# Kernel optimization log

Hardware: AMD Instinct MI355X
Metric: run time of the kernel (lower is better)

Reference implementation:

```python
import jax, jax.numpy as jnp
import numpy as np

NUM_HEADS = 8
D_HEAD = 16
RY = RX = 2
PH = 2 * RY + 1
PW = 2 * RX + 1
P = PH * PW  # 25 spatial positions per patch


def setup_inputs() -> dict:
    key = jax.random.key(0)
    ks = jax.random.split(key, 7)
    B, T, H, W, C = 1, 3, 96, 96, 128
    Ck = NUM_HEADS * D_HEAD
    w = lambda k, shp: jax.random.normal(k, shp, jnp.float32) * 0.05
    return {
        "x": jax.random.normal(ks[0], (B, T, H, W, C), jnp.float32),
        "Wq": w(ks[1], (C, Ck)),
        "Wk": w(ks[2], (C, Ck)),
        "Wv": w(ks[3], (C, Ck)),
        "Wo": w(ks[4], (Ck, C)),
        "temp_emb": w(ks[5], (T, Ck)),
        "sp_emb": w(ks[6], (P, Ck)),
    }


def _neighbor_idx(N, r):
    # Edge handling: patch center is clipped into the valid interior, matching
    # extract_patches(VALID) + gather_nd with clipped indices in the original.
    c = jnp.clip(jnp.arange(N), r, N - r - 1)
    return c[:, None] + jnp.arange(-r, r + 1)[None, :]  # (N, 2r+1)


def _query_spatial_idx(H, W):
    # Position of each query pixel inside its (clipped) patch.
    yc = jnp.clip(jnp.arange(H), RY, H - RY - 1)
    xc = jnp.clip(jnp.arange(W), RX, W - RX - 1)
    yr = jnp.arange(H) - yc + RY  # (H,)
    xr = jnp.arange(W) - xc + RX  # (W,)
    return yr[:, None] * PW + xr[None, :]  # (H, W) in [0, P)


def reference(x, Wq, Wk, Wv, Wo, temp_emb, sp_emb):
    B, T, H, W, C = x.shape
    h, d = NUM_HEADS, D_HEAD
    Ck = h * d
    # 1x1 conv projections (no bias) == channel matmuls
    Q = jnp.einsum('bqyxc,ck->bqyxk', x, Wq)
    K = jnp.einsum('bqyxc,ck->bqyxk', x, Wk)
    V = jnp.einsum('bqyxc,ck->bqyxk', x, Wv)
    # positional encodings added AFTER projection (attention space)
    K = K + temp_emb[None, :, None, None, :]
    qidx = _query_spatial_idx(H, W)  # (H, W)
    Q = Q + temp_emb[None, :, None, None, :] + sp_emb[qidx][None, None]
    # local spatial patch extraction with clipped-edge handling
    ynb = _neighbor_idx(H, RY)  # (H, PH)
    xnb = _neighbor_idx(W, RX)  # (W, PW)
    Kp = K[:, :, ynb[:, None, :, None], xnb[None, :, None, :], :]  # (B,T,H,W,PH,PW,Ck)
    Vp = V[:, :, ynb[:, None, :, None], xnb[None, :, None, :], :]
    Kp = Kp.reshape(B, T, H, W, P, Ck) + sp_emb[None, None, None, None]
    Vp = Vp.reshape(B, T, H, W, P, Ck)
    # merge key time into the neighborhood axis: (B,H,W,T*P,h,d)
    Kn = Kp.transpose(0, 2, 3, 1, 4, 5).reshape(B, H, W, T * P, h, d)
    Vn = Vp.transpose(0, 2, 3, 1, 4, 5).reshape(B, H, W, T * P, h, d)
    Qh = Q.reshape(B, T, H, W, h, d)
    scale = 1.0 / jnp.sqrt(jnp.asarray(d, x.dtype))
    scores = jnp.einsum('bqyxnd,byxknd->bqyxnk', Qh, Kn) * scale
    attn = jax.nn.softmax(scores, axis=-1)  # over T*P neighborhood
    out = jnp.einsum('bqyxnk,byxknd->bqyxnd', attn, Vn).reshape(B, T, H, W, Ck)
    out = jnp.einsum('bqyxk,kc->bqyxc', out, Wo)  # output 1x1 conv
    # return_list=False -> concatenate the T outputs along channels
    return out.transpose(0, 2, 3, 1, 4).reshape(B, H, W, T * C)
```

## Files before the change

kernel.cpp:

```cpp
#include <hip/hip_runtime.h>
#include <hip/hip_bf16.h>
#include <math.h>

#define TT 3
#define HH 96
#define WWD 96
#define CCH 128
#define NROWS (TT*HH*WWD)

typedef __attribute__((ext_vector_type(8))) short short8;
typedef __attribute__((ext_vector_type(4))) short short4v;
typedef __attribute__((ext_vector_type(4))) float float4v;

__device__ __forceinline__ float bfu(unsigned short u){ union{unsigned u;float f;}c; c.u=((unsigned)u)<<16; return c.f; }
__device__ __forceinline__ unsigned short f2bf(float f){ __hip_bfloat16 h=__float2bfloat16(f); return *(unsigned short*)&h; }

#if defined(__has_builtin)
#if __has_builtin(__builtin_amdgcn_mfma_f32_16x16x16bf16_1k)
#define MFMA16(A,B,C) __builtin_amdgcn_mfma_f32_16x16x16bf16_1k(A,B,C,0,0,0)
#endif
#endif
#ifndef MFMA16
static __device__ __forceinline__ float4v mfma16_asm(short4v a, short4v b, float4v c){
    float4v d;
    asm("v_mfma_f32_16x16x16_bf16 %0, %1, %2, %3" : "=v"(d) : "v"(a), "v"(b), "v"(c));
    return d;
}
#define MFMA16(A,B,C) mfma16_asm(A,B,C)
#endif

__launch_bounds__(256)
__global__ void prep_kernel(const float* __restrict__ Wq, const float* __restrict__ Wk,
                            const float* __restrict__ Wv, const float* __restrict__ Wo,
                            unsigned short* __restrict__ Wt, unsigned short* __restrict__ Wo1,
                            unsigned short* __restrict__ Wo2) {
    __shared__ float ts[32][33];
    const int m = blockIdx.x >> 4, tile = blockIdx.x & 15;
    const int k0 = (tile >> 2) * 32, n0 = (tile & 3) * 32;
    const float* src = (m == 0) ? Wq : (m == 1) ? Wk : (m == 2) ? Wv : Wo;
    const int tid = threadIdx.x;
    const int c = tid & 31, r8 = tid >> 5;
#pragma unroll
    for (int rr = 0; rr < 4; ++rr) {
        int r = r8 * 4 + rr;
        ts[r][c] = src[(size_t)(k0 + r) * 128 + n0 + c];
    }
    __syncthreads();
#pragma unroll
    for (int rr = 0; rr < 4; ++rr) {
        int r = r8 * 4 + rr;
        float v = ts[c][r];
        if (m < 3) {
            Wt[(size_t)(m * 128 + n0 + r) * 128 + k0 + c] = f2bf(v);
        } else {
            unsigned short w1 = f2bf(v);
            Wo1[(size_t)(n0 + r) * 128 + k0 + c] = w1;
            Wo2[(size_t)(n0 + r) * 128 + k0 + c] = f2bf(v - bfu(w1));
        }
    }
}

__launch_bounds__(256)
__global__ void qkv_kernel(const float* __restrict__ x,
                           const unsigned short* __restrict__ Wt,
                           const float* __restrict__ temp_emb,
                           const float* __restrict__ sp_emb,
                           unsigned short* __restrict__ Qb,
                           unsigned short* __restrict__ Kb,
                           unsigned short* __restrict__ Vb) {
    __shared__ unsigned short xs[32 * 136];
    const int tid = threadIdx.x;
    const int q0 = blockIdx.x * 32;
    for (int e = tid; e < 1024; e += 256) {
        int row = e >> 5, col = (e & 31) * 4;
        float4 v = *(const float4*)(x + (size_t)(q0 + row) * CCH + col);
        ushort4 u; u.x = f2bf(v.x); u.y = f2bf(v.y); u.z = f2bf(v.z); u.w = f2bf(v.w);
        *(ushort4*)&xs[row * 136 + col] = u;
    }
    __syncthreads();
    const int w = tid >> 6, lane = tid & 63, quad = lane >> 4, l16 = lane & 15;
    float4v acc[6][2];
#pragma unroll
    for (int mt = 0; mt < 6; ++mt)
#pragma unroll
        for (int nt = 0; nt < 2; ++nt) acc[mt][nt] = (float4v){0,0,0,0};
#pragma unroll
    for (int ks = 0; ks < 4; ++ks) {
        short8 b[2];
#pragma unroll
        for (int nt = 0; nt < 2; ++nt)
            b[nt] = *(const short8*)&xs[(nt * 16 + l16) * 136 + ks * 32 + quad * 8];
#pragma unroll
        for (int mt = 0; mt < 6; ++mt) {
            short8 a = *(const short8*)(Wt + (size_t)(w * 96 + mt * 16 + l16) * CCH + ks * 32 + quad * 8);
#pragma unroll
            for (int nt = 0; nt < 2; ++nt)
                acc[mt][nt] = __builtin_amdgcn_mfma_f32_16x16x32_bf16(a, b[nt], acc[mt][nt], 0, 0, 0);
        }
    }
#pragma unroll
    for (int nt = 0; nt < 2; ++nt) {
        int q = q0 + nt * 16 + l16;
        int t = q / (HH * WWD); int rem = q - t * (HH * WWD);
        int yy = rem / WWD, xx = rem - (rem / WWD) * WWD;
        int qidx = (yy - min(max(yy, 2), 93) + 2) * 5 + (xx - min(max(xx, 2), 93) + 2);
#pragma unroll
        for (int mt = 0; mt < 6; ++mt) {
            int colc = w * 96 + mt * 16 + quad * 4;
            int mat = colc >> 7, colb = colc & 127;
            float4v a = acc[mt][nt];
            ushort4 u;
            if (mat == 0) {
                float4 te = *(const float4*)(temp_emb + t * CCH + colb);
                float4 se = *(const float4*)(sp_emb + qidx * CCH + colb);
                u.x = f2bf((a[0] + te.x + se.x) * 0.25f);
                u.y = f2bf((a[1] + te.y + se.y) * 0.25f);
                u.z = f2bf((a[2] + te.z + se.z) * 0.25f);
                u.w = f2bf((a[3] + te.w + se.w) * 0.25f);
                *(ushort4*)(Qb + (size_t)q * CCH + colb) = u;
            } else if (mat == 1) {
                float4 te = *(const float4*)(temp_emb + t * CCH + colb);
                u.x = f2bf(a[0] + te.x); u.y = f2bf(a[1] + te.y);
                u.z = f2bf(a[2] + te.z); u.w = f2bf(a[3] + te.w);
                *(ushort4*)(Kb + (size_t)q * CCH + colb) = u;
            } else {
                u.x = f2bf(a[0]); u.y = f2bf(a[1]); u.z = f2bf(a[2]); u.w = f2bf(a[3]);
                *(ushort4*)(Vb + (size_t)q * CCH + colb) = u;
            }
        }
    }
}

#define PX 4
#define WIN 8

__launch_bounds__(512, 4)
__global__ void attn_kernel(const unsigned short* __restrict__ Qb,
                            const unsigned short* __restrict__ Kb,
                            const unsigned short* __restrict__ Vb,
                            const float* __restrict__ sp_emb,
                            const unsigned short* __restrict__ Wo1,
                            const unsigned short* __restrict__ Wo2,
                            float* __restrict__ out) {
    __shared__ unsigned short Ks[64 * 136];
    __shared__ unsigned short Vt[128 * 68];
    __shared__ float biasL[8 * 3 * 25 * 17];

    const int tid = threadIdx.x;
    const int lane = tid & 63;
    const int w = tid >> 6;
    const int quad = lane >> 4, l16 = lane & 15;
    const int h16 = w * 16;

    const int bx = blockIdx.x % (WWD / PX);
    const int by = blockIdx.x / (WWD / PX);
    const int x0 = bx * PX, y0 = by * PX;
    const int xlo = min(max(x0 - 2, 0), WWD - WIN);
    const int ylo = min(max(y0 - 2, 0), HH - WIN);

    const int qdy = l16 >> 2, qdx = l16 & 3;
    const int yy = y0 + qdy, xx = x0 + qdx;
    const int yc = min(max(yy, 2), HH - 3), xc = min(max(xx, 2), WWD - 3);

    short4v qfr[3];
#pragma unroll
    for (int qt = 0; qt < 3; ++qt) {
        int qrow = qt * (HH * WWD) + yy * WWD + xx;
        qfr[qt] = *(const short4v*)(Qb + (size_t)qrow * CCH + h16 + quad * 4);
    }

    short4v sph[2], spl[2];
#pragma unroll
    for (int tile = 0; tile < 2; ++tile) {
        int kcr = min(tile * 16 + l16, 24);
        float4 v = *(const float4*)(sp_emb + (size_t)kcr * CCH + h16 + quad * 4);
        float vv[4] = {v.x, v.y, v.z, v.w};
        union { short4v s4; unsigned short u[4]; } ph, pl;
#pragma unroll
        for (int i = 0; i < 4; ++i) {
            ph.u[i] = f2bf(vv[i]);
            pl.u[i] = f2bf(vv[i] - bfu(ph.u[i]));
        }
        sph[tile] = ph.s4; spl[tile] = pl.s4;
    }

    const int bbase = w * (3 * 25 * 17);
#pragma unroll
    for (int qt = 0; qt < 3; ++qt) {
#pragma unroll
        for (int tile = 0; tile < 2; ++tile) {
            float4v d = MFMA16(spl[tile], qfr[qt], ((float4v){0.f,0.f,0.f,0.f}));
            d = MFMA16(sph[tile], qfr[qt], d);
#pragma unroll
            for (int r = 0; r < 4; ++r) {
                int kc = tile * 16 + quad * 4 + r;
                if (kc < 25) biasL[bbase + (qt * 25 + kc) * 17 + l16] = d[r];
            }
        }
    }

    int badr[16];
#pragma unroll
    for (int kt = 0; kt < 4; ++kt)
#pragma unroll
        for (int r = 0; r < 4; ++r) {
            int slot = kt * 16 + quad * 4 + r;
            int gy = ylo + (slot >> 3), gx = xlo + (slot & 7);
            int py = gy - yc + 2, px = gx - xc + 2;
            bool ok = (py >= 0) && (py < 5) && (px >= 0) && (px < 5);
            badr[kt * 4 + r] = ok ? (bbase + (py * 5 + px) * 17 + l16) : -1;
        }

    float m[3] = {-1e30f, -1e30f, -1e30f};
    float l[3] = {0.f, 0.f, 0.f};
    float4v oacc[3];
#pragma unroll
    for (int qt = 0; qt < 3; ++qt) oacc[qt] = (float4v){0.f,0.f,0.f,0.f};

    for (int t = 0; t < TT; ++t) {
        __syncthreads();
        for (int e = tid; e < 1024; e += 512) {
            int slot = e >> 4, c = e & 15;
            int gy = ylo + (slot >> 3), gx = xlo + (slot & 7);
            size_t g = ((size_t)(t * HH + gy) * WWD + gx) * CCH + c * 8;
            *(uint4*)&Ks[slot * 136 + c * 8] = *(const uint4*)(Kb + g);
        }
        for (int p = tid; p < 1024; p += 512) {
            int sp2 = p & 31, cq = p >> 5;
            int slot0 = sp2 * 2, ch0 = cq * 4;
            int gy = ylo + (slot0 >> 3), gx = xlo + (slot0 & 7);
            size_t g = ((size_t)(t * HH + gy) * WWD + gx) * CCH + ch0;
            uint2 a = *(const uint2*)(Vb + g);
            uint2 b = *(const uint2*)(Vb + g + CCH);
            unsigned v0 = (a.x & 0xffffu) | (b.x << 16);
            unsigned v1 = (a.x >> 16)     | (b.x & 0xffff0000u);
            unsigned v2 = (a.y & 0xffffu) | (b.y << 16);
            unsigned v3 = (a.y >> 16)     | (b.y & 0xffff0000u);
            *(unsigned*)&Vt[(ch0 + 0) * 68 + slot0] = v0;
            *(unsigned*)&Vt[(ch0 + 1) * 68 + slot0] = v1;
            *(unsigned*)&Vt[(ch0 + 2) * 68 + slot0] = v2;
            *(unsigned*)&Vt[(ch0 + 3) * 68 + slot0] = v3;
        }
        __syncthreads();

        short4v kfr[4], vfr[4];
#pragma unroll
        for (int kt = 0; kt < 4; ++kt) {
            kfr[kt] = *(const short4v*)&Ks[(kt * 16 + l16) * 136 + h16 + quad * 4];
            vfr[kt] = *(const short4v*)&Vt[(h16 + l16) * 68 + kt * 16 + quad * 4];
        }

#pragma unroll
        for (int qt = 0; qt < 3; ++qt) {
            float4v s[4];
#pragma unroll
            for (int kt = 0; kt < 4; ++kt) {
                float4v c;
#pragma unroll
                for (int r = 0; r < 4; ++r) {
                    int a = badr[kt * 4 + r];
                    c[r] = (a < 0) ? -1e30f : biasL[a + qt * 425];
                }
                s[kt] = MFMA16(kfr[kt], qfr[qt], c);
            }
            float mx = m[qt];
#pragma unroll
            for (int kt = 0; kt < 4; ++kt)
#pragma unroll
                for (int r = 0; r < 4; ++r) mx = fmaxf(mx, s[kt][r]);
            mx = fmaxf(mx, __shfl_xor(mx, 16));
            mx = fmaxf(mx, __shfl_xor(mx, 32));
            float corr = __expf(m[qt] - mx);
            m[qt] = mx;
            l[qt] *= corr;
            float4v oc = oacc[qt] * corr;
            float lsum = 0.f;
            short4v pfr[4];
#pragma unroll
            for (int kt = 0; kt < 4; ++kt) {
                float p0 = __expf(s[kt][0] - mx), p1 = __expf(s[kt][1] - mx);
                float p2 = __expf(s[kt][2] - mx), p3 = __expf(s[kt][3] - mx);
                lsum += (p0 + p1) + (p2 + p3);
                union { short4v s4; unsigned short u[4]; } pk;
                pk.u[0] = f2bf(p0); pk.u[1] = f2bf(p1);
                pk.u[2] = f2bf(p2); pk.u[3] = f2bf(p3);
                pfr[kt] = pk.s4;
            }
            l[qt] += lsum;
#pragma unroll
            for (int kt = 0; kt < 4; ++kt) oc = MFMA16(vfr[kt], pfr[kt], oc);
            oacc[qt] = oc;
        }
    }

    __syncthreads();
    unsigned short* Os = Ks;
#pragma unroll
    for (int qt = 0; qt < 3; ++qt) {
        float lt = l[qt];
        lt += __shfl_xor(lt, 16);
        lt += __shfl_xor(lt, 32);
        float inv = 1.f / lt;
        union { ushort4 u4; unsigned short u[4]; } ob;
#pragma unroll
        for (int r = 0; r < 4; ++r) ob.u[r] = f2bf(oacc[qt][r] * inv);
        *(ushort4*)&Os[(qt * 16 + l16) * 136 + h16 + quad * 4] = ob.u4;
    }
    __syncthreads();

    float4v pacc[3];
#pragma unroll
    for (int nt = 0; nt < 3; ++nt) pacc[nt] = (float4v){0.f, 0.f, 0.f, 0.f};
#pragma unroll
    for (int ks = 0; ks < 4; ++ks) {
        short8 bfrag[3];
#pragma unroll
        for (int nt = 0; nt < 3; ++nt)
            bfrag[nt] = *(const short8*)&Os[(nt * 16 + l16) * 136 + ks * 32 + quad * 8];
        size_t wo = (size_t)(w * 16 + l16) * CCH + ks * 32 + quad * 8;
        short8 a1 = *(const short8*)(Wo1 + wo);
        short8 a2 = *(const short8*)(Wo2 + wo);
#pragma unroll
        for (int nt = 0; nt < 3; ++nt) {
            pacc[nt] = __builtin_amdgcn_mfma_f32_16x16x32_bf16(a1, bfrag[nt], pacc[nt], 0, 0, 0);
            pacc[nt] = __builtin_amdgcn_mfma_f32_16x16x32_bf16(a2, bfrag[nt], pacc[nt], 0, 0, 0);
        }
    }
#pragma unroll
    for (int nt = 0; nt < 3; ++nt) {
        size_t ob = ((size_t)(yy * WWD + xx) * TT + nt) * CCH;
        float4 o;
        o.x = pacc[nt][0]; o.y = pacc[nt][1]; o.z = pacc[nt][2]; o.w = pacc[nt][3];
        *(float4*)(out + ob + w * 16 + quad * 4) = o;
    }
}

extern "C" void kernel_launch(void* const* d_in, const int* in_sizes, int n_in,
                              void* d_out, int out_size, void* d_ws, size_t ws_size,
                              hipStream_t stream) {
    const float* x        = (const float*)d_in[0];
    const float* Wq       = (const float*)d_in[1];
    const float* Wk       = (const float*)d_in[2];
    const float* Wv       = (const float*)d_in[3];
    const float* Wo       = (const float*)d_in[4];
    const float* temp_emb = (const float*)d_in[5];
    const float* sp_emb   = (const float*)d_in[6];
    float* out = (float*)d_out;

    const size_t nb = (size_t)NROWS * CCH * 2;
    unsigned short* Qb  = (unsigned short*)d_ws;
    unsigned short* Kb  = (unsigned short*)((char*)d_ws + nb);
    unsigned short* Vb  = (unsigned short*)((char*)d_ws + 2 * nb);
    unsigned short* Wt  = (unsigned short*)((char*)d_ws + 3 * nb);
    unsigned short* Wo1 = Wt + 384 * 128;
    unsigned short* Wo2 = Wo1 + 128 * 128;

    prep_kernel<<<64, 256, 0, stream>>>(Wq, Wk, Wv, Wo, Wt, Wo1, Wo2);
    qkv_kernel<<<NROWS / 32, 256, 0, stream>>>(x, Wt, temp_emb, sp_emb, Qb, Kb, Vb);
    attn_kernel<<<(HH / PX) * (WWD / PX), 512, 0, stream>>>(Qb, Kb, Vb, sp_emb, Wo1, Wo2, out);
}
```

Baseline: 144.8 us.

## Load K fragments directly from global and use per-wave V transpose slabs

K MFMA fragments are now read straight from global memory by each wave instead of being staged through a block-wide shared tile. The V transpose moves into per-wave, per-head shared slabs, double-buffered by time step. That removes both block-level __syncthreads per time step, and the time loop is fully unrolled. In exchange each wave issues more scattered global loads, and correctness relies on intra-wave ordering of the slab writes and reads with no explicit barrier.

```diff
diff --git a/kernel.cpp b/kernel.cpp
--- a/kernel.cpp
+++ b/kernel.cpp
@@ -133,6 +133,8 @@
 
 #define PX 4
 #define WIN 8
+#define VSTR 68
+#define VSLAB (16*VSTR)
 
 __launch_bounds__(512, 4)
 __global__ void attn_kernel(const unsigned short* __restrict__ Qb,
@@ -142,9 +144,10 @@
                             const unsigned short* __restrict__ Wo1,
                             const unsigned short* __restrict__ Wo2,
                             float* __restrict__ out) {
-    __shared__ unsigned short Ks[64 * 136];
-    __shared__ unsigned short Vt[128 * 68];
-    __shared__ float biasL[8 * 3 * 25 * 17];
+    __shared__ __align__(16) char smem[40800 + 2 * 8 * VSLAB * 2];
+    float* biasL = (float*)smem;
+    unsigned short* VtA = (unsigned short*)(smem + 40800);
+    unsigned short* Os  = (unsigned short*)(smem + 40800);
 
     const int tid = threadIdx.x;
     const int lane = tid & 63;
@@ -217,38 +220,41 @@
 #pragma unroll
     for (int qt = 0; qt < 3; ++qt) oacc[qt] = (float4v){0.f,0.f,0.f,0.f};
 
+#pragma unroll
     for (int t = 0; t < TT; ++t) {
-        __syncthreads();
-        for (int e = tid; e < 1024; e += 512) {
-            int slot = e >> 4, c = e & 15;
+        short4v kfr[4];
+#pragma unroll
+        for (int kt = 0; kt < 4; ++kt) {
+            int slot = kt * 16 + l16;
             int gy = ylo + (slot >> 3), gx = xlo + (slot & 7);
-            size_t g = ((size_t)(t * HH + gy) * WWD + gx) * CCH + c * 8;
-            *(uint4*)&Ks[slot * 136 + c * 8] = *(const uint4*)(Kb + g);
-        }
-        for (int p = tid; p < 1024; p += 512) {
-            int sp2 = p & 31, cq = p >> 5;
-            int slot0 = sp2 * 2, ch0 = cq * 4;
+            size_t g = ((size_t)(t * HH + gy) * WWD + gx) * CCH + h16 + quad * 4;
+            kfr[kt] = *(const short4v*)(Kb + g);
+        }
+
+        unsigned short* vt = VtA + ((size_t)((t & 1) * 8 + w)) * VSLAB;
+#pragma unroll
+        for (int r = 0; r < 2; ++r) {
+            int task = r * 64 + lane;
+            int sp2 = task & 31, c4 = task >> 5;
+            int slot0 = sp2 * 2, ch0 = c4 * 4;
             int gy = ylo + (slot0 >> 3), gx = xlo + (slot0 & 7);
-            size_t g = ((size_t)(t * HH + gy) * WWD + gx) * CCH + ch0;
+            size_t g = ((size_t)(t * HH + gy) * WWD + gx) * CCH + h16 + ch0;
             uint2 a = *(const uint2*)(Vb + g);
             uint2 b = *(const uint2*)(Vb + g + CCH);
             unsigned v0 = (a.x & 0xffffu) | (b.x << 16);
             unsigned v1 = (a.x >> 16)     | (b.x & 0xffff0000u);
             unsigned v2 = (a.y & 0xffffu) | (b.y << 16);
             unsigned v3 = (a.y >> 16)     | (b.y & 0xffff0000u);
-            *(unsigned*)&Vt[(ch0 + 0) * 68 + slot0] = v0;
-            *(unsigned*)&Vt[(ch0 + 1) * 68 + slot0] = v1;
-            *(unsigned*)&Vt[(ch0 + 2) * 68 + slot0] = v2;
-            *(unsigned*)&Vt[(ch0 + 3) * 68 + slot0] = v3;
-        }
-        __syncthreads();
-
-        short4v kfr[4], vfr[4];
-#pragma unroll
-        for (int kt = 0; kt < 4; ++kt) {
-            kfr[kt] = *(const short4v*)&Ks[(kt * 16 + l16) * 136 + h16 + quad * 4];
-            vfr[kt] = *(const short4v*)&Vt[(h16 + l16) * 68 + kt * 16 + quad * 4];
-        }
+            *(unsigned*)&vt[(ch0 + 0) * VSTR + slot0] = v0;
+            *(unsigned*)&vt[(ch0 + 1) * VSTR + slot0] = v1;
+            *(unsigned*)&vt[(ch0 + 2) * VSTR + slot0] = v2;
+            *(unsigned*)&vt[(ch0 + 3) * VSTR + slot0] = v3;
+        }
+
+        short4v vfr[4];
+#pragma unroll
+        for (int kt = 0; kt < 4; ++kt)
+            vfr[kt] = *(const short4v*)&vt[l16 * VSTR + kt * 16 + quad * 4];
 
 #pragma unroll
         for (int qt = 0; qt < 3; ++qt) {
@@ -294,7 +300,6 @@
     }
 
     __syncthreads();
-    unsigned short* Os = Ks;
 #pragma unroll
     for (int qt = 0; qt < 3; ++qt) {
         float lt = l[qt];
```

Result: slower. 200.4 us (+38.4%).

## Double-buffer K/V tiles across time steps and hoist attention bias into registers

Applied to the files above, without the earlier changes.

The attention kernel now prefetches the next time step's K and V neighborhood into registers while the current step computes. It then writes them into a second LDS buffer, so each time step needs one barrier instead of two. The positional bias for all three query times is gathered from LDS into registers once, before the loop, rather than being re-read from LDS inside each score MFMA. The bias, staging and output buffers now share one aliased LDS allocation, which is smaller than before. The register-resident bias and prefetch values add a lot of register pressure under launch_bounds(512,4), which risks spills or reduced occupancy.

```diff
diff --git a/kernel.cpp b/kernel.cpp
--- a/kernel.cpp
+++ b/kernel.cpp
@@ -133,6 +133,8 @@
 
 #define PX 4
 #define WIN 8
+#define KHS 8704
+#define VHS 8704
 
 __launch_bounds__(512, 4)
 __global__ void attn_kernel(const unsigned short* __restrict__ Qb,
@@ -142,9 +144,11 @@
                             const unsigned short* __restrict__ Wo1,
                             const unsigned short* __restrict__ Wo2,
                             float* __restrict__ out) {
-    __shared__ unsigned short Ks[64 * 136];
-    __shared__ unsigned short Vt[128 * 68];
-    __shared__ float biasL[8 * 3 * 25 * 17];
+    __shared__ __align__(16) char smem[2 * KHS * 2 + 2 * VHS * 2];
+    unsigned short* KsA = (unsigned short*)smem;
+    unsigned short* VtA = (unsigned short*)(smem + 2 * KHS * 2);
+    float* biasL = (float*)smem;
+    unsigned short* Os = (unsigned short*)smem;
 
     const int tid = threadIdx.x;
     const int lane = tid & 63;
@@ -162,6 +166,55 @@
     const int yy = y0 + qdy, xx = x0 + qdx;
     const int yc = min(max(yy, 2), HH - 3), xc = min(max(xx, 2), WWD - 3);
 
+    uint4 kreg[2];
+    uint2 var[2], vbr[2];
+
+    auto stage_load = [&](int t) {
+#pragma unroll
+        for (int i = 0; i < 2; ++i) {
+            int e = i * 512 + tid;
+            int slot = e >> 4, c = e & 15;
+            int gy = ylo + (slot >> 3), gx = xlo + (slot & 7);
+            size_t g = ((size_t)(t * HH + gy) * WWD + gx) * CCH + c * 8;
+            kreg[i] = *(const uint4*)(Kb + g);
+        }
+#pragma unroll
+        for (int i = 0; i < 2; ++i) {
+            int p = i * 512 + tid;
+            int sp2 = p & 31, cq = p >> 5;
+            int slot0 = sp2 * 2;
+            int gy = ylo + (slot0 >> 3), gx = xlo + (slot0 & 7);
+            size_t g = ((size_t)(t * HH + gy) * WWD + gx) * CCH + cq * 4;
+            var[i] = *(const uint2*)(Vb + g);
+            vbr[i] = *(const uint2*)(Vb + g + CCH);
+        }
+    };
+    auto stage_write = [&](unsigned short* Kd, unsigned short* Vd) {
+#pragma unroll
+        for (int i = 0; i < 2; ++i) {
+            int e = i * 512 + tid;
+            int slot = e >> 4, c = e & 15;
+            *(uint4*)&Kd[slot * 136 + c * 8] = kreg[i];
+        }
+#pragma unroll
+        for (int i = 0; i < 2; ++i) {
+            int p = i * 512 + tid;
+            int sp2 = p & 31, cq = p >> 5;
+            int slot0 = sp2 * 2, ch0 = cq * 4;
+            uint2 a = var[i], b = vbr[i];
+            unsigned v0 = (a.x & 0xffffu) | (b.x << 16);
+            unsigned v1 = (a.x >> 16)     | (b.x & 0xffff0000u);
+            unsigned v2 = (a.y & 0xffffu) | (b.y << 16);
+            unsigned v3 = (a.y >> 16)     | (b.y & 0xffff0000u);
+            *(unsigned*)&Vd[(ch0 + 0) * 68 + slot0] = v0;
+            *(unsigned*)&Vd[(ch0 + 1) * 68 + slot0] = v1;
+            *(unsigned*)&Vd[(ch0 + 2) * 68 + slot0] = v2;
+            *(unsigned*)&Vd[(ch0 + 3) * 68 + slot0] = v3;
+        }
+    };
+
+    stage_load(0);
+
     short4v qfr[3];
 #pragma unroll
     for (int qt = 0; qt < 3; ++qt) {
@@ -199,7 +252,7 @@
         }
     }
 
-    int badr[16];
+    float4v cbias[3][4];
 #pragma unroll
     for (int kt = 0; kt < 4; ++kt)
 #pragma unroll
@@ -208,8 +261,15 @@
             int gy = ylo + (slot >> 3), gx = xlo + (slot & 7);
             int py = gy - yc + 2, px = gx - xc + 2;
             bool ok = (py >= 0) && (py < 5) && (px >= 0) && (px < 5);
-            badr[kt * 4 + r] = ok ? (bbase + (py * 5 + px) * 17 + l16) : -1;
-        }
+            int a = ok ? (bbase + (py * 5 + px) * 17 + l16) : -1;
+#pragma unroll
+            for (int qt = 0; qt < 3; ++qt)
+                cbias[qt][kt][r] = (a < 0) ? -1e30f : biasL[a + qt * 425];
+        }
+
+    __syncthreads();
+    stage_write(KsA, VtA);
+    __syncthreads();
 
     float m[3] = {-1e30f, -1e30f, -1e30f};
     float l[3] = {0.f, 0.f, 0.f};
@@ -217,52 +277,26 @@
 #pragma unroll
     for (int qt = 0; qt < 3; ++qt) oacc[qt] = (float4v){0.f,0.f,0.f,0.f};
 
+#pragma unroll
     for (int t = 0; t < TT; ++t) {
-        __syncthreads();
-        for (int e = tid; e < 1024; e += 512) {
-            int slot = e >> 4, c = e & 15;
-            int gy = ylo + (slot >> 3), gx = xlo + (slot & 7);
-            size_t g = ((size_t)(t * HH + gy) * WWD + gx) * CCH + c * 8;
-            *(uint4*)&Ks[slot * 136 + c * 8] = *(const uint4*)(Kb + g);
-        }
-        for (int p = tid; p < 1024; p += 512) {
-            int sp2 = p & 31, cq = p >> 5;
-            int slot0 = sp2 * 2, ch0 = cq * 4;
-            int gy = ylo + (slot0 >> 3), gx = xlo + (slot0 & 7);
-            size_t g = ((size_t)(t * HH + gy) * WWD + gx) * CCH + ch0;
-            uint2 a = *(const uint2*)(Vb + g);
-            uint2 b = *(const uint2*)(Vb + g + CCH);
-            unsigned v0 = (a.x & 0xffffu) | (b.x << 16);
-            unsigned v1 = (a.x >> 16)     | (b.x & 0xffff0000u);
-            unsigned v2 = (a.y & 0xffffu) | (b.y << 16);
-            unsigned v3 = (a.y >> 16)     | (b.y & 0xffff0000u);
-            *(unsigned*)&Vt[(ch0 + 0) * 68 + slot0] = v0;
-            *(unsigned*)&Vt[(ch0 + 1) * 68 + slot0] = v1;
-            *(unsigned*)&Vt[(ch0 + 2) * 68 + slot0] = v2;
-            *(unsigned*)&Vt[(ch0 + 3) * 68 + slot0] = v3;
-        }
-        __syncthreads();
+        if (t + 1 < TT) stage_load(t + 1);
+
+        const unsigned short* Kc = KsA + (t & 1) * KHS;
+        const unsigned short* Vc = VtA + (t & 1) * VHS;
 
         short4v kfr[4], vfr[4];
 #pragma unroll
         for (int kt = 0; kt < 4; ++kt) {
-            kfr[kt] = *(const short4v*)&Ks[(kt * 16 + l16) * 136 + h16 + quad * 4];
-            vfr[kt] = *(const short4v*)&Vt[(h16 + l16) * 68 + kt * 16 + quad * 4];
+            kfr[kt] = *(const short4v*)&Kc[(kt * 16 + l16) * 136 + h16 + quad * 4];
+            vfr[kt] = *(const short4v*)&Vc[(h16 + l16) * 68 + kt * 16 + quad * 4];
         }
 
 #pragma unroll
         for (int qt = 0; qt < 3; ++qt) {
             float4v s[4];
 #pragma unroll
-            for (int kt = 0; kt < 4; ++kt) {
-                float4v c;
-#pragma unroll
-                for (int r = 0; r < 4; ++r) {
-                    int a = badr[kt * 4 + r];
-                    c[r] = (a < 0) ? -1e30f : biasL[a + qt * 425];
-                }
-                s[kt] = MFMA16(kfr[kt], qfr[qt], c);
-            }
+            for (int kt = 0; kt < 4; ++kt)
+                s[kt] = MFMA16(kfr[kt], qfr[qt], cbias[qt][kt]);
             float mx = m[qt];
 #pragma unroll
             for (int kt = 0; kt < 4; ++kt)
@@ -291,10 +325,12 @@
             for (int kt = 0; kt < 4; ++kt) oc = MFMA16(vfr[kt], pfr[kt], oc);
             oacc[qt] = oc;
         }
-    }
-
-    __syncthreads();
-    unsigned short* Os = Ks;
+
+        if (t + 1 < TT)
+            stage_write(KsA + ((t + 1) & 1) * KHS, VtA + ((t + 1) & 1) * VHS);
+        __syncthreads();
+    }
+
 #pragma unroll
     for (int qt = 0; qt < 3; ++qt) {
         float lt = l[qt];
```

Result: slower. 188.1 us (+29.9%).
